# Optimization experiments

Hardware: AMD Instinct MI355X
Metric: run time of the kernel (lower is better)

## Reference

```python
import jax, jax.numpy as jnp
import numpy as np

N_HEADS = 12


def setup_inputs() -> dict:
    key = jax.random.key(0)
    ks = jax.random.split(key, 4)
    B, T, C = 1, 4096, 768
    x = jax.random.normal(ks[0], (B, T, C), dtype=jnp.float32)
    w_qkv = jax.random.normal(ks[1], (C, 3 * C), dtype=jnp.float32) * (C ** -0.5)
    b_qkv = jnp.zeros((3 * C,), dtype=jnp.float32)
    w_proj = jax.random.normal(ks[2], (C, C), dtype=jnp.float32) * (C ** -0.5)
    b_proj = jnp.zeros((C,), dtype=jnp.float32)
    return {"x": x, "w_qkv": w_qkv, "b_qkv": b_qkv, "w_proj": w_proj, "b_proj": b_proj}


def reference(x, w_qkv, b_qkv, w_proj, b_proj):
    B, T, C = x.shape
    H = N_HEADS
    hd = C // H
    qkv = x @ w_qkv + b_qkv                      # [B,T,3C]
    q, k, v = jnp.split(qkv, 3, axis=-1)
    # [B,H,T,hd]
    q = q.reshape(B, T, H, hd).transpose(0, 2, 1, 3)
    k = k.reshape(B, T, H, hd).transpose(0, 2, 1, 3)
    v = v.reshape(B, T, H, hd).transpose(0, 2, 1, 3)
    scale = 1.0 / jnp.sqrt(jnp.float32(hd))
    attn = jnp.einsum('bhqd,bhkd->bhqk', q, k) * scale  # [B,H,T,T]
    causal = jnp.tril(jnp.ones((T, T), dtype=bool))
    attn = jnp.where(causal, attn, jnp.float32(-jnp.inf))
    attn = jax.nn.softmax(attn, axis=-1)
    out = jnp.einsum('bhqk,bhkd->bhqd', attn, v)        # [B,H,T,hd]
    out = out.transpose(0, 2, 1, 3).reshape(B, T, C)
    return out @ w_proj + b_proj
```

## Files before the change

kernel.cpp:

```cpp
#include <hip/hip_runtime.h>
#include <hip/hip_bf16.h>


#define T_SEQ 4096
#define C_DIM 768
#define C3    2304
#define NH    12
#define HD    64

typedef __attribute__((ext_vector_type(8))) short bf16x8;
typedef __attribute__((ext_vector_type(4))) short bf16x4;
typedef __attribute__((ext_vector_type(4))) float f32x4;

__device__ inline unsigned short f2bf(float f) {
  union { float f; unsigned u; } v; v.f = f;
  unsigned r = v.u + 0x7fff + ((v.u >> 16) & 1);
  return (unsigned short)(r >> 16);
}
__device__ inline unsigned short f2bf_trunc(float f) {
  union { float f; unsigned u; } v; v.f = f;
  return (unsigned short)(v.u >> 16);
}

__device__ inline void gl2lds16(const void* g, void* l) {
  __builtin_amdgcn_global_load_lds(
      (const __attribute__((address_space(1))) unsigned int*)g,
      (__attribute__((address_space(3))) unsigned int*)l, 16, 0, 0);
}

#if __has_builtin(__builtin_amdgcn_exp2f)
#define EXP2F(x) __builtin_amdgcn_exp2f(x)
#else
#define EXP2F(x) exp2f(x)
#endif

#define NB_CONV  (T_SEQ * C_DIM / 2048)
#define NB_TQKV  ((C3 / 32) * (C_DIM / 32))
#define NB_TPROJ ((C_DIM / 32) * (C_DIM / 32))

__global__ __launch_bounds__(256) void prep_fused(
    const float* __restrict__ x, const float* __restrict__ w_qkv,
    const float* __restrict__ w_proj, unsigned short* __restrict__ xb,
    unsigned short* __restrict__ wqkvT, unsigned short* __restrict__ wprojT) {
  __shared__ float t[32][33];
  const int b = blockIdx.x;
  const int tid = threadIdx.x;

  if (b < NB_CONV) {
    int i = (b * 256 + tid) * 8;
    float4 v0 = *(const float4*)(x + i);
    float4 v1 = *(const float4*)(x + i + 4);
    unsigned short o[8] = {f2bf(v0.x), f2bf(v0.y), f2bf(v0.z), f2bf(v0.w),
                           f2bf(v1.x), f2bf(v1.y), f2bf(v1.z), f2bf(v1.w)};
    *(uint4*)(xb + i) = *(uint4*)o;
    return;
  }
  const float* in;
  unsigned short* outT;
  int R, Cc, bi;
  if (b < NB_CONV + NB_TQKV) {
    in = w_qkv; outT = wqkvT; R = C_DIM; Cc = C3; bi = b - NB_CONV;
  } else {
    in = w_proj; outT = wprojT; R = C_DIM; Cc = C_DIM; bi = b - NB_CONV - NB_TQKV;
  }
  const int tx = tid & 31, ty = tid >> 5;
  const int c0 = (bi % (Cc / 32)) * 32, r0 = (bi / (Cc / 32)) * 32;
#pragma unroll
  for (int i = 0; i < 4; ++i) {
    int r = ty + i * 8;
    t[r][tx] = in[(size_t)(r0 + r) * Cc + c0 + tx];
  }
  __syncthreads();
#pragma unroll
  for (int i = 0; i < 4; ++i) {
    int c = ty + i * 8;
    outT[(size_t)(c0 + c) * R + r0 + tx] = f2bf(t[tx][c]);
  }
}

__global__ __launch_bounds__(512) void gemm_qkv(
    const unsigned short* __restrict__ A, const unsigned short* __restrict__ Bt,
    const float* __restrict__ bias, unsigned short* __restrict__ Cq,
    unsigned short* __restrict__ vTp, int M, int N, int K) {
  __shared__ unsigned short As[256 * 64];
  __shared__ unsigned short Bs[128 * 64];
  const int tid = threadIdx.x;
  const int wave = tid >> 6, lane = tid & 63;
  const int lo = lane & 15, g8 = lane >> 4;
  const int lo7 = lo & 7;
  const int wm = wave >> 1, wn = wave & 1;
  const int bm = blockIdx.y * 256, bn = blockIdx.x * 128;
  const int drow = tid >> 3;
  const int dslot = (tid & 7) * 8;
  const int dsrc = ((tid & 7) ^ (drow & 7)) * 8;

  f32x4 acc[4][4];
#pragma unroll
  for (int mt = 0; mt < 4; ++mt)
#pragma unroll
    for (int nt = 0; nt < 4; ++nt) acc[mt][nt] = (f32x4){0.f, 0.f, 0.f, 0.f};

  const unsigned short* Abase = A + (size_t)bm * K;
  const unsigned short* Bbase = Bt + (size_t)bn * K;

  for (int k0 = 0; k0 < K; k0 += 64) {
    __syncthreads();
#pragma unroll
    for (int p = 0; p < 4; ++p) {
      const int r = p * 64 + drow;
      gl2lds16(Abase + (size_t)r * K + k0 + dsrc, As + r * 64 + dslot);
    }
#pragma unroll
    for (int p = 0; p < 2; ++p) {
      const int r = p * 64 + drow;
      gl2lds16(Bbase + (size_t)r * K + k0 + dsrc, Bs + r * 64 + dslot);
    }
    __syncthreads();

#pragma unroll
    for (int kk = 0; kk < 2; ++kk) {
      bf16x8 a[4], b[4];
#pragma unroll
      for (int mt = 0; mt < 4; ++mt)
        a[mt] = *(const bf16x8*)(
            As + (wm * 64 + mt * 16 + lo) * 64 + (((kk * 4 + g8) ^ lo7) * 8));
#pragma unroll
      for (int nt = 0; nt < 4; ++nt)
        b[nt] = *(const bf16x8*)(
            Bs + (wn * 64 + nt * 16 + lo) * 64 + (((kk * 4 + g8) ^ lo7) * 8));
#pragma unroll
      for (int mt = 0; mt < 4; ++mt)
#pragma unroll
        for (int nt = 0; nt < 4; ++nt)
          acc[mt][nt] = __builtin_amdgcn_mfma_f32_16x16x32_bf16(a[mt], b[nt], acc[mt][nt], 0, 0, 0);
    }
  }

  if (bn < 2 * C_DIM) {
    const float sc = (bn < C_DIM) ? 0.18033688011112042f : 1.0f;
#pragma unroll
    for (int nt = 0; nt < 4; ++nt) {
      const int n = bn + wn * 64 + nt * 16 + lo;
      const float bv = bias[n];
#pragma unroll
      for (int mt = 0; mt < 4; ++mt)
#pragma unroll
        for (int r = 0; r < 4; ++r) {
          const int m = bm + wm * 64 + mt * 16 + g8 * 4 + r;
          Cq[(size_t)m * C3 + n] = f2bf((acc[mt][nt][r] + bv) * sc);
        }
    }
  } else {
#pragma unroll
    for (int nt = 0; nt < 4; ++nt) {
      const int n = bn + wn * 64 + nt * 16 + lo;
      const float bv = bias[n];
      unsigned short* row = vTp + (size_t)(n - 2 * C_DIM) * T_SEQ;
#pragma unroll
      for (int mt = 0; mt < 4; ++mt) {
        const int mbase = (bm + wm * 64 + mt * 16 + g8 * 4) & ~31;
        bf16x4 o4;
#pragma unroll
        for (int r = 0; r < 4; ++r) o4[r] = (short)f2bf(acc[mt][nt][r] + bv);
        *(bf16x4*)(row + mbase + 8 * g8 + 4 * (mt & 1)) = o4;
      }
    }
  }
}

__global__ __launch_bounds__(256) void gemm_bt_mfma(
    const unsigned short* __restrict__ A, const unsigned short* __restrict__ Bt,
    const float* __restrict__ bias, float* __restrict__ C,
    int M, int N, int K) {
  __shared__ unsigned short As[128 * 64];
  __shared__ unsigned short Bs[128 * 64];
  const int tid = threadIdx.x;
  const int wave = tid >> 6, lane = tid & 63;
  const int lo = lane & 15, g8 = lane >> 4;
  const int lo7 = lo & 7;
  const int wm = wave >> 1, wn = wave & 1;
  const int bm = blockIdx.y * 128, bn = blockIdx.x * 128;
  const int drow8 = lane >> 3;
  const int dslot = (lane & 7) * 8;
  const int dsrc = ((lane & 7) ^ drow8) * 8;

  f32x4 acc[4][4];
#pragma unroll
  for (int mt = 0; mt < 4; ++mt)
#pragma unroll
    for (int nt = 0; nt < 4; ++nt) acc[mt][nt] = (f32x4){0.f, 0.f, 0.f, 0.f};

  const unsigned short* Abase = A + (size_t)bm * K;
  const unsigned short* Bbase = Bt + (size_t)bn * K;

  for (int k0 = 0; k0 < K; k0 += 64) {
    __syncthreads();
#pragma unroll
    for (int p = 0; p < 4; ++p) {
      const int r = p * 32 + wave * 8 + drow8;
      gl2lds16(Abase + (size_t)r * K + k0 + dsrc, As + r * 64 + dslot);
      gl2lds16(Bbase + (size_t)r * K + k0 + dsrc, Bs + r * 64 + dslot);
    }
    __syncthreads();

#pragma unroll
    for (int kk = 0; kk < 2; ++kk) {
      bf16x8 a[4], b[4];
#pragma unroll
      for (int mt = 0; mt < 4; ++mt)
        a[mt] = *(const bf16x8*)(
            As + (wm * 64 + mt * 16 + lo) * 64 + (((kk * 4 + g8) ^ lo7) * 8));
#pragma unroll
      for (int nt = 0; nt < 4; ++nt)
        b[nt] = *(const bf16x8*)(
            Bs + (wn * 64 + nt * 16 + lo) * 64 + (((kk * 4 + g8) ^ lo7) * 8));
#pragma unroll
      for (int mt = 0; mt < 4; ++mt)
#pragma unroll
        for (int nt = 0; nt < 4; ++nt)
          acc[mt][nt] = __builtin_amdgcn_mfma_f32_16x16x32_bf16(a[mt], b[nt], acc[mt][nt], 0, 0, 0);
    }
  }

#pragma unroll
  for (int nt = 0; nt < 4; ++nt) {
    const int n = bn + wn * 64 + nt * 16 + lo;
    const float bv = bias[n];
#pragma unroll
    for (int mt = 0; mt < 4; ++mt)
#pragma unroll
      for (int r = 0; r < 4; ++r) {
        const int m = bm + wm * 64 + mt * 16 + g8 * 4 + r;
        C[(size_t)m * N + n] = acc[mt][nt][r] + bv;
      }
  }
}

#define NRECH  51
#define PO_REC (256 * 64)
#define KSTEP  (64 * C3)

__device__ inline int s_pref(int qt) {
  const int A = qt / 3, B = qt - 3 * A;
  return qt + 3 * A * (A - 1) / 2 + A * B;
}

__global__ __launch_bounds__(512) void flash_attn_ksplit(
    const unsigned short* __restrict__ qkv,
    const unsigned short* __restrict__ vTp,
    float* __restrict__ Po, float* __restrict__ Pl) {
  __shared__ unsigned short Ks[3][64 * 64];
  __shared__ unsigned short Vs[3][64 * 64];

  const int u = blockIdx.x;
  int h, qt, c, k0, T;
  if (u < 480) {
    h = u / 40;
    const int w40 = u % 40;
    qt = 2; c = 0;
    for (int q = 15; q >= 2; --q) {
      const int A = q / 3, B = q - 3 * A;
      const int F = 3 * A * (A - 1) / 2 + A * (B + 1);
      if (w40 >= F) { qt = q; c = w40 - F; break; }
    }
    k0 = 12 * c; T = 12;
  } else if (u < 540) {
    const int v = u - 480; h = v / 5; const int e = v % 5;
    qt = 3 * e + 1; c = e; k0 = 12 * e; T = 8;
  } else {
    const int v = u - 540; h = v / 6; const int e = v % 6;
    qt = 3 * e; c = e; k0 = 12 * e; T = 4;
  }
  const int rec = h * NRECH + s_pref(qt) + c;
  const int qt4 = 4 * qt;

  const int tid = threadIdx.x;
  const int w = tid >> 6;
  const int qg = w >> 1;
  const int kg = w & 1;
  const int lane = tid & 63;
  const int lo = lane & 15;
  const int g = lane >> 4;
  const int lo7 = lo & 7;

  const unsigned short* Kg = qkv + C_DIM + h * HD;
  const unsigned short* Vg = vTp + (size_t)(h * HD) * T_SEQ;

  const int drow = tid >> 3;
  const int dslot = (tid & 7) * 8;
  const int dsrc = ((tid & 7) ^ (drow & 7)) * 8;

  bf16x8 qb[4][2];
#pragma unroll
  for (int qh = 0; qh < 4; ++qh)
#pragma unroll
    for (int dh = 0; dh < 2; ++dh)
      qb[qh][dh] = *(const bf16x8*)(
          qkv + (size_t)(qt * 256 + qg * 64 + qh * 16 + lo) * C3 + h * HD + dh * 32 + g * 8);

  const unsigned short* pK = Kg + (size_t)(k0 * 64 + drow) * C3 + dsrc;
  const unsigned short* pV = Vg + (size_t)drow * T_SEQ + k0 * 64 + dsrc;

  auto stage = [&](int buf) __attribute__((always_inline)) {
    gl2lds16(pK, Ks[buf] + drow * 64 + dslot);
    gl2lds16(pV, Vs[buf] + drow * 64 + dslot);
    pK += KSTEP; pV += 64;
  };

  stage(0);
  stage(1);
  asm volatile("s_waitcnt vmcnt(2)" ::: "memory");
  __builtin_amdgcn_s_barrier();

  f32x4 o_acc[4][4];
  float l_i[4];
#pragma unroll
  for (int qh = 0; qh < 4; ++qh) {
    l_i[qh] = 0.f;
#pragma unroll
    for (int dt = 0; dt < 4; ++dt) o_acc[qh][dt] = (f32x4){0.f, 0.f, 0.f, 0.f};
  }

  int ic = 0, iw = 2;
  int ktc = k0;
  for (int t = 0; t < T; ++t) {
    if (t + 2 < T) stage(iw);
    const unsigned short* Kc = Ks[ic];
    const unsigned short* Vc = Vs[ic];

    bf16x8 af[2][2], av[4];
#pragma unroll
    for (int mt = 0; mt < 2; ++mt)
#pragma unroll
      for (int dh = 0; dh < 2; ++dh)
        af[mt][dh] = *(const bf16x8*)(
            Kc + (kg * 32 + mt * 16 + lo) * 64 + (((dh * 4 + g) ^ lo7) * 8));
#pragma unroll
    for (int dt = 0; dt < 4; ++dt)
      av[dt] = *(const bf16x8*)(
          Vc + (dt * 16 + lo) * 64 + (((kg * 4 + g) ^ lo7) * 8));

    const bool diag = (ktc >= qt4);
    const int mb = (ktc - qt4) * 64 + kg * 32;

    __builtin_amdgcn_s_setprio(1);
#pragma unroll
    for (int qh = 0; qh < 4; ++qh) {
      f32x4 st0 = (f32x4){0.f, 0.f, 0.f, 0.f};
      f32x4 st1 = (f32x4){0.f, 0.f, 0.f, 0.f};
#pragma unroll
      for (int dh = 0; dh < 2; ++dh) {
        st0 = __builtin_amdgcn_mfma_f32_16x16x32_bf16(af[0][dh], qb[qh][dh], st0, 0, 0, 0);
        st1 = __builtin_amdgcn_mfma_f32_16x16x32_bf16(af[1][dh], qb[qh][dh], st1, 0, 0, 0);
      }
      if (diag) {
        const int qr = qg * 64 + qh * 16 + lo;
#pragma unroll
        for (int r = 0; r < 4; ++r) {
          if (mb + g * 4 + r > qr) st0[r] = -1e30f;
          if (mb + 16 + g * 4 + r > qr) st1[r] = -1e30f;
        }
      }
      bf16x8 pb;
      float ls = 0.f;
#pragma unroll
      for (int jj = 0; jj < 4; ++jj) {
        float e0 = EXP2F(st0[jj]);
        float e1 = EXP2F(st1[jj]);
        ls += e0 + e1;
        pb[jj] = (short)f2bf_trunc(e0);
        pb[4 + jj] = (short)f2bf_trunc(e1);
      }
      l_i[qh] += ls;
#pragma unroll
      for (int dt = 0; dt < 4; ++dt)
        o_acc[qh][dt] = __builtin_amdgcn_mfma_f32_16x16x32_bf16(
            av[dt], pb, o_acc[qh][dt], 0, 0, 0);
    }
    __builtin_amdgcn_s_setprio(0);

    if (t + 2 < T)
      asm volatile("s_waitcnt vmcnt(2)" ::: "memory");
    else
      asm volatile("s_waitcnt vmcnt(0)" ::: "memory");
    __builtin_amdgcn_s_barrier();

    ic = (ic == 2) ? 0 : ic + 1;
    iw = (iw == 2) ? 0 : iw + 1;
    ++ktc;
  }

#pragma unroll
  for (int qh = 0; qh < 4; ++qh) {
    l_i[qh] += __shfl_xor(l_i[qh], 16);
    l_i[qh] += __shfl_xor(l_i[qh], 32);
  }
  float* red = (float*)Ks[0];
#pragma unroll
  for (int p = 0; p < 4; ++p) {
    if (qg == p && kg == 1) {
#pragma unroll
      for (int qh = 0; qh < 4; ++qh) {
#pragma unroll
        for (int dt = 0; dt < 4; ++dt)
          *(f32x4*)(red + (qh * 16 + lo) * 64 + dt * 16 + g * 4) = o_acc[qh][dt];
        if (g == 0) red[4096 + qh * 16 + lo] = l_i[qh];
      }
    }
    __syncthreads();
    if (qg == p && kg == 0) {
#pragma unroll
      for (int qh = 0; qh < 4; ++qh) {
#pragma unroll
        for (int dt = 0; dt < 4; ++dt) {
          f32x4 v = *(const f32x4*)(red + (qh * 16 + lo) * 64 + dt * 16 + g * 4);
          o_acc[qh][dt] += v;
        }
        l_i[qh] += red[4096 + qh * 16 + lo];
      }
    }
    __syncthreads();
  }

  if (kg == 0) {
    float* PoS = Po + (size_t)rec * PO_REC;
#pragma unroll
    for (int qh = 0; qh < 4; ++qh)
#pragma unroll
      for (int dt = 0; dt < 4; ++dt)
        *(f32x4*)(PoS + (qg * 64 + qh * 16 + lo) * 64 + dt * 16 + g * 4) =
            o_acc[qh][dt];
    if (g == 0) {
      float* PlS = Pl + (size_t)rec * 256;
#pragma unroll
      for (int qh = 0; qh < 4; ++qh) PlS[qg * 64 + qh * 16 + lo] = l_i[qh];
    }
  }
}

__global__ __launch_bounds__(256) void combine_qb256(
    const float* __restrict__ Po, const float* __restrict__ Pl,
    unsigned short* __restrict__ out) {
  const int bid = blockIdx.x;
  const int h = bid / 32;
  const int r2 = bid % 32;
  const int qt = r2 >> 1, half = r2 & 1;
  const int nc = qt / 3 + 1;
  const int rec0 = h * NRECH + s_pref(qt);
  const int tid = threadIdx.x;
  const int q0 = tid >> 2;
  const int c0 = (tid & 3) * 16;
#pragma unroll
  for (int qq = 0; qq < 2; ++qq) {
    const int q = (half * 2 + qq) * 64 + q0;
    float l = 0.f;
    f32x4 acc[4];
#pragma unroll
    for (int e = 0; e < 4; ++e) acc[e] = (f32x4){0.f, 0.f, 0.f, 0.f};
    for (int c = 0; c < nc; ++c) {
      const size_t base = (size_t)(rec0 + c);
      l += Pl[base * 256 + q];
      const float* P = Po + base * PO_REC + q * 64 + c0;
#pragma unroll
      for (int e = 0; e < 4; ++e) acc[e] += *(const f32x4*)(P + e * 4);
    }
    const float inv = 1.0f / l;
    unsigned short ob[16];
#pragma unroll
    for (int e = 0; e < 4; ++e)
#pragma unroll
      for (int r = 0; r < 4; ++r) ob[e * 4 + r] = f2bf(acc[e][r] * inv);
    unsigned short* op = out + (size_t)(qt * 256 + q) * C_DIM + h * 64 + c0;
    *(uint4*)op = *(uint4*)ob;
    *(uint4*)(op + 8) = *(uint4*)(ob + 8);
  }
}

extern "C" void kernel_launch(void* const* d_in, const int* in_sizes, int n_in,
                              void* d_out, int out_size, void* d_ws, size_t ws_size,
                              hipStream_t stream) {
  const float* x      = (const float*)d_in[0];
  const float* w_qkv  = (const float*)d_in[1];
  const float* b_qkv  = (const float*)d_in[2];
  const float* w_proj = (const float*)d_in[3];
  const float* b_proj = (const float*)d_in[4];
  float* out = (float*)d_out;

  unsigned short* xb     = (unsigned short*)d_ws;
  unsigned short* wqkvT  = xb + (size_t)T_SEQ * C_DIM;
  unsigned short* wprojT = wqkvT + (size_t)C3 * C_DIM;
  unsigned short* qkv    = wprojT + (size_t)C_DIM * C_DIM;
  unsigned short* vTp    = qkv + (size_t)T_SEQ * C3;
  unsigned short* attnb  = xb;
  float* Po = (float*)(vTp + (size_t)C_DIM * T_SEQ);
  float* Pl = Po + (size_t)NH * NRECH * PO_REC;

  prep_fused<<<NB_CONV + NB_TQKV + NB_TPROJ, 256, 0, stream>>>(
      x, w_qkv, w_proj, xb, wqkvT, wprojT);

  gemm_qkv<<<dim3(C3 / 128, T_SEQ / 256), 512, 0, stream>>>(
      xb, wqkvT, b_qkv, qkv, vTp, T_SEQ, C3, C_DIM);

  flash_attn_ksplit<<<612, 512, 0, stream>>>(qkv, vTp, Po, Pl);

  combine_qb256<<<NH * 16 * 2, 256, 0, stream>>>(Po, Pl, attnb);

  gemm_bt_mfma<<<dim3(C_DIM / 128, T_SEQ / 128), 256, 0, stream>>>(
      attnb, wprojT, b_proj, out, T_SEQ, C_DIM, C_DIM);
}
```

Measured before the change: 195.5 us.

## Use 4 fat waves per attention block, removing intra-block K-split reduction

The flash attention kernel drops from 8 waves (4 query groups × 2 key halves) to 4 waves, with each wave handling both 32-key halves of every 64-key tile. This removes the LDS-based cross-wave reduction of partial outputs and its barriers at the end. Each thread now issues twice the staging loads, and the wait counts are adjusted to match. The cost is half as many waves per block, so less latency hiding per CU, and more serial MFMA work per wave.

Measured after the change: 185.1 us. -5.3%, faster.

```diff
diff --git a/kernel.cpp b/kernel.cpp
--- a/kernel.cpp
+++ b/kernel.cpp
@@ -245,7 +245,7 @@
   return qt + 3 * A * (A - 1) / 2 + A * B;
 }
 
-__global__ __launch_bounds__(512) void flash_attn_ksplit(
+__global__ __launch_bounds__(256) void flash_attn_fat4(
     const unsigned short* __restrict__ qkv,
     const unsigned short* __restrict__ vTp,
     float* __restrict__ Po, float* __restrict__ Pl) {
@@ -275,9 +275,7 @@
   const int qt4 = 4 * qt;
 
   const int tid = threadIdx.x;
-  const int w = tid >> 6;
-  const int qg = w >> 1;
-  const int kg = w & 1;
+  const int qg = tid >> 6;
   const int lane = tid & 63;
   const int lo = lane & 15;
   const int g = lane >> 4;
@@ -298,18 +296,22 @@
       qb[qh][dh] = *(const bf16x8*)(
           qkv + (size_t)(qt * 256 + qg * 64 + qh * 16 + lo) * C3 + h * HD + dh * 32 + g * 8);
 
-  const unsigned short* pK = Kg + (size_t)(k0 * 64 + drow) * C3 + dsrc;
-  const unsigned short* pV = Vg + (size_t)drow * T_SEQ + k0 * 64 + dsrc;
+  const unsigned short* pK0 = Kg + (size_t)(k0 * 64 + drow) * C3 + dsrc;
+  const unsigned short* pK1 = pK0 + (size_t)32 * C3;
+  const unsigned short* pV0 = Vg + (size_t)drow * T_SEQ + k0 * 64 + dsrc;
+  const unsigned short* pV1 = pV0 + (size_t)32 * T_SEQ;
 
   auto stage = [&](int buf) __attribute__((always_inline)) {
-    gl2lds16(pK, Ks[buf] + drow * 64 + dslot);
-    gl2lds16(pV, Vs[buf] + drow * 64 + dslot);
-    pK += KSTEP; pV += 64;
+    gl2lds16(pK0, Ks[buf] + drow * 64 + dslot);
+    gl2lds16(pK1, Ks[buf] + (32 + drow) * 64 + dslot);
+    gl2lds16(pV0, Vs[buf] + drow * 64 + dslot);
+    gl2lds16(pV1, Vs[buf] + (32 + drow) * 64 + dslot);
+    pK0 += KSTEP; pK1 += KSTEP; pV0 += 64; pV1 += 64;
   };
 
   stage(0);
   stage(1);
-  asm volatile("s_waitcnt vmcnt(2)" ::: "memory");
+  asm volatile("s_waitcnt vmcnt(4)" ::: "memory");
   __builtin_amdgcn_s_barrier();
 
   f32x4 o_acc[4][4];
@@ -328,59 +330,63 @@
     const unsigned short* Kc = Ks[ic];
     const unsigned short* Vc = Vs[ic];
 
-    bf16x8 af[2][2], av[4];
-#pragma unroll
-    for (int mt = 0; mt < 2; ++mt)
-#pragma unroll
-      for (int dh = 0; dh < 2; ++dh)
-        af[mt][dh] = *(const bf16x8*)(
-            Kc + (kg * 32 + mt * 16 + lo) * 64 + (((dh * 4 + g) ^ lo7) * 8));
-#pragma unroll
-    for (int dt = 0; dt < 4; ++dt)
-      av[dt] = *(const bf16x8*)(
-          Vc + (dt * 16 + lo) * 64 + (((kg * 4 + g) ^ lo7) * 8));
-
     const bool diag = (ktc >= qt4);
-    const int mb = (ktc - qt4) * 64 + kg * 32;
-
-    __builtin_amdgcn_s_setprio(1);
-#pragma unroll
-    for (int qh = 0; qh < 4; ++qh) {
-      f32x4 st0 = (f32x4){0.f, 0.f, 0.f, 0.f};
-      f32x4 st1 = (f32x4){0.f, 0.f, 0.f, 0.f};
-#pragma unroll
-      for (int dh = 0; dh < 2; ++dh) {
-        st0 = __builtin_amdgcn_mfma_f32_16x16x32_bf16(af[0][dh], qb[qh][dh], st0, 0, 0, 0);
-        st1 = __builtin_amdgcn_mfma_f32_16x16x32_bf16(af[1][dh], qb[qh][dh], st1, 0, 0, 0);
+
+#pragma unroll
+    for (int kh = 0; kh < 2; ++kh) {
+      bf16x8 af[2][2], av[4];
+#pragma unroll
+      for (int mt = 0; mt < 2; ++mt)
+#pragma unroll
+        for (int dh = 0; dh < 2; ++dh)
+          af[mt][dh] = *(const bf16x8*)(
+              Kc + (kh * 32 + mt * 16 + lo) * 64 + (((dh * 4 + g) ^ lo7) * 8));
+#pragma unroll
+      for (int dt = 0; dt < 4; ++dt)
+        av[dt] = *(const bf16x8*)(
+            Vc + (dt * 16 + lo) * 64 + (((kh * 4 + g) ^ lo7) * 8));
+
+      const int mb = (ktc - qt4) * 64 + kh * 32;
+
+      __builtin_amdgcn_s_setprio(1);
+#pragma unroll
+      for (int qh = 0; qh < 4; ++qh) {
+        f32x4 st0 = (f32x4){0.f, 0.f, 0.f, 0.f};
+        f32x4 st1 = (f32x4){0.f, 0.f, 0.f, 0.f};
+#pragma unroll
+        for (int dh = 0; dh < 2; ++dh) {
+          st0 = __builtin_amdgcn_mfma_f32_16x16x32_bf16(af[0][dh], qb[qh][dh], st0, 0, 0, 0);
+          st1 = __builtin_amdgcn_mfma_f32_16x16x32_bf16(af[1][dh], qb[qh][dh], st1, 0, 0, 0);
+        }
+        if (diag) {
+          const int qr = qg * 64 + qh * 16 + lo;
+#pragma unroll
+          for (int r = 0; r < 4; ++r) {
+            if (mb + g * 4 + r > qr) st0[r] = -1e30f;
+            if (mb + 16 + g * 4 + r > qr) st1[r] = -1e30f;
+          }
+        }
+        bf16x8 pb;
+        float ls = 0.f;
+#pragma unroll
+        for (int jj = 0; jj < 4; ++jj) {
+          float e0 = EXP2F(st0[jj]);
+          float e1 = EXP2F(st1[jj]);
+          ls += e0 + e1;
+          pb[jj] = (short)f2bf_trunc(e0);
+          pb[4 + jj] = (short)f2bf_trunc(e1);
+        }
+        l_i[qh] += ls;
+#pragma unroll
+        for (int dt = 0; dt < 4; ++dt)
+          o_acc[qh][dt] = __builtin_amdgcn_mfma_f32_16x16x32_bf16(
+              av[dt], pb, o_acc[qh][dt], 0, 0, 0);
       }
-      if (diag) {
-        const int qr = qg * 64 + qh * 16 + lo;
-#pragma unroll
-        for (int r = 0; r < 4; ++r) {
-          if (mb + g * 4 + r > qr) st0[r] = -1e30f;
-          if (mb + 16 + g * 4 + r > qr) st1[r] = -1e30f;
-        }
-      }
-      bf16x8 pb;
-      float ls = 0.f;
-#pragma unroll
-      for (int jj = 0; jj < 4; ++jj) {
-        float e0 = EXP2F(st0[jj]);
-        float e1 = EXP2F(st1[jj]);
-        ls += e0 + e1;
-        pb[jj] = (short)f2bf_trunc(e0);
-        pb[4 + jj] = (short)f2bf_trunc(e1);
-      }
-      l_i[qh] += ls;
-#pragma unroll
-      for (int dt = 0; dt < 4; ++dt)
-        o_acc[qh][dt] = __builtin_amdgcn_mfma_f32_16x16x32_bf16(
-            av[dt], pb, o_acc[qh][dt], 0, 0, 0);
-    }
-    __builtin_amdgcn_s_setprio(0);
+      __builtin_amdgcn_s_setprio(0);
+    }
 
     if (t + 2 < T)
-      asm volatile("s_waitcnt vmcnt(2)" ::: "memory");
+      asm volatile("s_waitcnt vmcnt(4)" ::: "memory");
     else
       asm volatile("s_waitcnt vmcnt(0)" ::: "memory");
     __builtin_amdgcn_s_barrier();
@@ -395,46 +401,17 @@
     l_i[qh] += __shfl_xor(l_i[qh], 16);
     l_i[qh] += __shfl_xor(l_i[qh], 32);
   }
-  float* red = (float*)Ks[0];
-#pragma unroll
-  for (int p = 0; p < 4; ++p) {
-    if (qg == p && kg == 1) {
-#pragma unroll
-      for (int qh = 0; qh < 4; ++qh) {
-#pragma unroll
-        for (int dt = 0; dt < 4; ++dt)
-          *(f32x4*)(red + (qh * 16 + lo) * 64 + dt * 16 + g * 4) = o_acc[qh][dt];
-        if (g == 0) red[4096 + qh * 16 + lo] = l_i[qh];
-      }
-    }
-    __syncthreads();
-    if (qg == p && kg == 0) {
-#pragma unroll
-      for (int qh = 0; qh < 4; ++qh) {
-#pragma unroll
-        for (int dt = 0; dt < 4; ++dt) {
-          f32x4 v = *(const f32x4*)(red + (qh * 16 + lo) * 64 + dt * 16 + g * 4);
-          o_acc[qh][dt] += v;
-        }
-        l_i[qh] += red[4096 + qh * 16 + lo];
-      }
-    }
-    __syncthreads();
-  }
-
-  if (kg == 0) {
-    float* PoS = Po + (size_t)rec * PO_REC;
-#pragma unroll
-    for (int qh = 0; qh < 4; ++qh)
-#pragma unroll
-      for (int dt = 0; dt < 4; ++dt)
-        *(f32x4*)(PoS + (qg * 64 + qh * 16 + lo) * 64 + dt * 16 + g * 4) =
-            o_acc[qh][dt];
-    if (g == 0) {
-      float* PlS = Pl + (size_t)rec * 256;
-#pragma unroll
-      for (int qh = 0; qh < 4; ++qh) PlS[qg * 64 + qh * 16 + lo] = l_i[qh];
-    }
+  float* PoS = Po + (size_t)rec * PO_REC;
+#pragma unroll
+  for (int qh = 0; qh < 4; ++qh)
+#pragma unroll
+    for (int dt = 0; dt < 4; ++dt)
+      *(f32x4*)(PoS + (qg * 64 + qh * 16 + lo) * 64 + dt * 16 + g * 4) =
+          o_acc[qh][dt];
+  if (g == 0) {
+    float* PlS = Pl + (size_t)rec * 256;
+#pragma unroll
+    for (int qh = 0; qh < 4; ++qh) PlS[qg * 64 + qh * 16 + lo] = l_i[qh];
   }
 }
 
@@ -501,7 +478,7 @@
   gemm_qkv<<<dim3(C3 / 128, T_SEQ / 256), 512, 0, stream>>>(
       xb, wqkvT, b_qkv, qkv, vTp, T_SEQ, C3, C_DIM);
 
-  flash_attn_ksplit<<<612, 512, 0, stream>>>(qkv, vTp, Po, Pl);
+  flash_attn_fat4<<<612, 256, 0, stream>>>(qkv, vTp, Po, Pl);
 
   combine_qb256<<<NH * 16 * 2, 256, 0, stream>>>(Po, Pl, attnb);
 
```
